# Kernel tuning notes

Hardware: AMD Instinct MI355X
Metric: run time of the kernel (lower is better)

## Reference

```python
import jax, jax.numpy as jnp
import numpy as np

DIM = 1024
HEADS = 16
HEAD_DIM = DIM // HEADS
N_CLUSTERS = 8
B, N = 4, 1024


def setup_inputs() -> dict:
    key = jax.random.key(0)
    ks = jax.random.split(key, 10)
    s = 0.02
    return {
        "x": jax.random.normal(ks[0], (B, N, DIM), dtype=jnp.float32),
        "Wqkv": jax.random.normal(ks[1], (DIM, 3 * DIM), dtype=jnp.float32) * s,
        "Wproj": jax.random.normal(ks[2], (DIM, DIM), dtype=jnp.float32) * s,
        "bproj": jnp.zeros((DIM,), dtype=jnp.float32),
        "Wgroup": jax.random.normal(ks[3], (HEAD_DIM, N_CLUSTERS), dtype=jnp.float32) * s,
        "bgroup": jnp.zeros((N_CLUSTERS,), dtype=jnp.float32),
        "Wtheta": jax.random.normal(ks[4], (HEAD_DIM, 1), dtype=jnp.float32) * s,
        "btheta": jnp.zeros((1,), dtype=jnp.float32),
        "affinity_B": jax.random.normal(ks[5], (HEADS, N_CLUSTERS, N_CLUSTERS), dtype=jnp.float32),
        "cp_bias_scale": jnp.asarray(1.0, dtype=jnp.float32),
        "flag": 1,
        "injection": 0,
        "cp_dcmm": 1,
    }


def reference(x, Wqkv, Wproj, bproj, Wgroup, bgroup, Wtheta, btheta,
              affinity_B, cp_bias_scale, flag, injection, cp_dcmm):
    b, n, c = x.shape
    h = affinity_B.shape[0]
    hd = c // h
    scale = hd ** -0.5
    # qkv: [b,n,3c] -> [3,b,h,n,hd]
    qkv = (x @ Wqkv).reshape(b, n, 3, h, hd).transpose(2, 0, 3, 1, 4)
    q, k, v = qkv[0], qkv[1], qkv[2]
    attn = jnp.einsum('bhnd,bhmd->bhnm', q, k) * scale
    z_constraint = jnp.asarray(0.0, dtype=x.dtype)
    if cp_dcmm and flag:
        # cluster assignments per query token
        z = jax.nn.softmax(q @ Wgroup + bgroup, axis=-1)          # [b,h,n,K]
        B_aff = jax.nn.sigmoid(affinity_B)                         # [h,K,K]
        zB = jnp.einsum('bhik,hkl->bhil', z, B_aff)
        cp_bias_ori = jnp.tanh(jnp.einsum('bhil,bhjl->bhij', zB, z))  # [b,h,n,n]
        theta = jax.nn.relu(jnp.squeeze(q @ Wtheta + btheta, -1))  # [b,h,n]
        degree_term = theta[..., :, None] * theta[..., None, :]
        cp_bias = cp_bias_scale * degree_term * cp_bias_ori
        attn = attn + cp_bias
        z_constraint = -(z * jnp.log(z + 1e-8)).sum(axis=-1).mean()
    else:
        cp_bias = jnp.zeros_like(attn)
    attn = jax.nn.softmax(attn, axis=-1)
    out = jnp.einsum('bhnm,bhmd->bhnd', attn, v).transpose(0, 2, 1, 3).reshape(b, n, c)
    out = out @ Wproj + bproj
    zero = jnp.asarray(0.0, dtype=x.dtype)
    return (out, z_constraint, zero, zero, cp_bias)
```

## Files before the change

### kernel.cpp

```cpp
#include <hip/hip_runtime.h>
#include <stdint.h>

#define DIM 1024
#define HEADS 16
#define HD 64
#define NC 8
#define BB 4
#define NN 1024
#define ROWS (BB*NN)
#define TOK (BB*HEADS*NN)
#define OUT_OFF_Z (ROWS*DIM)
#define CP_OFF    (ROWS*DIM+3)

typedef __bf16 bf16_t;
typedef __attribute__((ext_vector_type(8))) __bf16 bf16x8;
typedef __attribute__((ext_vector_type(4))) __bf16 bf16x4;
typedef __attribute__((ext_vector_type(4))) float f32x4;

__device__ __forceinline__ void gload16(const void* g, void* l){
#if __has_builtin(__builtin_amdgcn_global_load_lds)
  __builtin_amdgcn_global_load_lds(
      (__attribute__((address_space(1))) void*)(g),
      (__attribute__((address_space(3))) void*)(l), 16, 0, 0);
#else
  *(uint4*)l = *(const uint4*)g;
#endif
}

__global__ __launch_bounds__(256) void prep_small(const float* __restrict__ affB,
                                                  float* __restrict__ sigB,
                                                  float* __restrict__ out_scalars){
  int i = blockIdx.x*256 + threadIdx.x;
  if(i < HEADS*NC*NC) sigB[i] = 1.f/(1.f + __expf(-affB[i]));
  if(i < 3) out_scalars[i] = 0.f;
}

__global__ __launch_bounds__(256) void cvt_bf16(const float* __restrict__ in,
                                                bf16_t* __restrict__ out){
  int i = (blockIdx.x*256 + threadIdx.x)*4;
  float4 v = *(const float4*)&in[i];
  bf16x4 o = {(bf16_t)v.x, (bf16_t)v.y, (bf16_t)v.z, (bf16_t)v.w};
  *(bf16x4*)&out[i] = o;
}

__global__ __launch_bounds__(256) void transpose_bf16(const float* __restrict__ in,
                                                      bf16_t* __restrict__ out,
                                                      int K, int N){
  __shared__ float tile[32][33];
  int k0 = blockIdx.y*32, n0 = blockIdx.x*32;
  int tx = threadIdx.x & 31, ty = threadIdx.x >> 5;
  #pragma unroll
  for(int r=ty; r<32; r+=8) tile[r][tx] = in[(size_t)(k0+r)*N + n0+tx];
  __syncthreads();
  #pragma unroll
  for(int r=ty; r<32; r+=8) out[(size_t)(n0+r)*K + k0+tx] = (bf16_t)tile[tx][r];
}

__global__ __launch_bounds__(256) void gemm_qkv(const bf16_t* __restrict__ A,
                                                const bf16_t* __restrict__ Bt,
                                                bf16_t* __restrict__ Qb,
                                                bf16_t* __restrict__ Kb,
                                                bf16_t* __restrict__ Vt){
  const int K = DIM;
  __shared__ __align__(16) bf16_t As[128*32];
  __shared__ __align__(16) bf16_t Bs[128*32];
  const int tid  = threadIdx.x;
  const int m0 = blockIdx.y*128, n0 = blockIdx.x*128;
  const int wave = tid>>6, lane = tid&63, l15 = lane&15, quad = lane>>4;
  const int wm = (wave>>1)*64, wn = (wave&1)*64;

  f32x4 acc[4][4];
  #pragma unroll
  for(int i=0;i<4;i++)
    #pragma unroll
    for(int j=0;j<4;j++) acc[i][j] = (f32x4){0.f,0.f,0.f,0.f};

  for(int k0=0; k0<K; k0+=32){
    int c = tid;
    gload16(A  + (size_t)(m0 + (c>>2))*K + k0 + (c&3)*8, &As[c*8]);
    gload16(Bt + (size_t)(n0 + (c>>2))*K + k0 + (c&3)*8, &Bs[c*8]);
    c = tid + 256;
    gload16(A  + (size_t)(m0 + (c>>2))*K + k0 + (c&3)*8, &As[c*8]);
    gload16(Bt + (size_t)(n0 + (c>>2))*K + k0 + (c&3)*8, &Bs[c*8]);
    __syncthreads();

    bf16x8 a[4], b[4];
    #pragma unroll
    for(int i=0;i<4;i++) a[i] = *(const bf16x8*)&As[(wm + i*16 + l15)*32 + quad*8];
    #pragma unroll
    for(int j=0;j<4;j++) b[j] = *(const bf16x8*)&Bs[(wn + j*16 + l15)*32 + quad*8];
    #pragma unroll
    for(int i=0;i<4;i++)
      #pragma unroll
      for(int j=0;j<4;j++)
        acc[i][j] = __builtin_amdgcn_mfma_f32_16x16x32_bf16(a[i], b[j], acc[i][j], 0,0,0);
    __syncthreads();
  }

  #pragma unroll
  for(int j=0;j<4;j++){
    int col = n0 + wn + j*16 + l15;
    int which = col>>10, hc = col&1023, h = hc>>6, d = hc&63;
    #pragma unroll
    for(int i=0;i<4;i++){
      int m = m0 + wm + i*16 + quad*4;
      #pragma unroll
      for(int r=0;r<4;r++){
        int row = m + r;
        int bh = (row>>10)*HEADS + h, n = row&1023;
        bf16_t v = (bf16_t)acc[i][j][r];
        if(which==0)      Qb[((size_t)bh*NN + n)*HD + d] = v;
        else if(which==1) Kb[((size_t)bh*NN + n)*HD + d] = v;
        else              Vt[((size_t)bh*HD + d)*NN + n] = v;
      }
    }
  }
}

__global__ __launch_bounds__(256) void token_kernel(
    const bf16_t* __restrict__ Qb, const float* __restrict__ Wgroup,
    const float* __restrict__ bgroup, const float* __restrict__ Wtheta,
    const float* __restrict__ btheta, const float* __restrict__ sigB,
    bf16_t* __restrict__ zb16, bf16_t* __restrict__ zBb16,
    float* __restrict__ thetaAll, float* __restrict__ entPart){
  const int wv = threadIdx.x>>6, lane = threadIdx.x&63;
  const int t = blockIdx.x*4 + wv;
  const int h = (t>>10)&15;
  float qd = (float)Qb[(size_t)t*HD + lane];

  float zl[8];
  #pragma unroll
  for(int c=0;c<8;c++){
    float p = qd * Wgroup[lane*NC + c];
    p += __shfl_xor(p,1);  p += __shfl_xor(p,2);  p += __shfl_xor(p,4);
    p += __shfl_xor(p,8);  p += __shfl_xor(p,16); p += __shfl_xor(p,32);
    zl[c] = p + bgroup[c];
  }
  float th = qd * Wtheta[lane];
  th += __shfl_xor(th,1);  th += __shfl_xor(th,2);  th += __shfl_xor(th,4);
  th += __shfl_xor(th,8);  th += __shfl_xor(th,16); th += __shfl_xor(th,32);
  th = fmaxf(th + btheta[0], 0.f);

  float mx = zl[0];
  #pragma unroll
  for(int c=1;c<8;c++) mx = fmaxf(mx, zl[c]);
  float ssum = 0.f;
  #pragma unroll
  for(int c=0;c<8;c++){ zl[c] = __expf(zl[c]-mx); ssum += zl[c]; }
  float inv = 1.f/ssum;
  float ent = 0.f;
  #pragma unroll
  for(int c=0;c<8;c++){ float z = zl[c]*inv; zl[c] = z; ent -= z*__logf(z + 1e-8f); }

  float zb[8];
  #pragma unroll
  for(int l=0;l<8;l++){
    float a = 0.f;
    #pragma unroll
    for(int k2=0;k2<8;k2++) a += zl[k2]*sigB[h*64 + k2*8 + l];
    zb[l] = a;
  }
  if(lane==0){
    bf16x8 zv, zbv;
    #pragma unroll
    for(int c=0;c<8;c++){ zv[c] = (bf16_t)zl[c]; zbv[c] = (bf16_t)zb[c]; }
    *(bf16x8*)&zb16[(size_t)t*8]  = zv;
    *(bf16x8*)&zBb16[(size_t)t*8] = zbv;
    thetaAll[t] = th;
  }

  __shared__ float es[4];
  if(lane==0) es[wv] = ent;
  __syncthreads();
  if(threadIdx.x==0) entPart[blockIdx.x] = es[0]+es[1]+es[2]+es[3];
}

__global__ __launch_bounds__(256) void reduce_ent(const float* __restrict__ part,
                                                  float* __restrict__ outz){
  float s = 0.f;
  for(int i=threadIdx.x; i<TOK/4; i+=256) s += part[i];
  s += __shfl_xor(s,1); s += __shfl_xor(s,2); s += __shfl_xor(s,4);
  s += __shfl_xor(s,8); s += __shfl_xor(s,16); s += __shfl_xor(s,32);
  __shared__ float ls[4];
  if((threadIdx.x&63)==0) ls[threadIdx.x>>6] = s;
  __syncthreads();
  if(threadIdx.x==0) outz[0] = (ls[0]+ls[1]+ls[2]+ls[3]) * (1.0f/(float)TOK);
}

__global__ __launch_bounds__(256) void flash_kernel(
    const bf16_t* __restrict__ Qb, const bf16_t* __restrict__ Kb,
    const bf16_t* __restrict__ Vt, const bf16_t* __restrict__ zb16,
    const bf16_t* __restrict__ zBb16, const float* __restrict__ thetaAll,
    const float* __restrict__ cps_p, float* __restrict__ cp_out,
    bf16_t* __restrict__ attnO){
  const int bid = blockIdx.x;
  const int bh = bid & 63, qt = bid >> 6;
  const int b = bh >> 4;
  const int tid = threadIdx.x;
  const int wave = tid>>6, lane = tid&63, l15 = lane&15, quad = lane>>4;

  __shared__ __align__(16) bf16_t Qs[64*64];
  __shared__ __align__(16) bf16_t Ks[64*64];
  __shared__ __align__(16) bf16_t Vs[64*64];
  __shared__ __align__(16) bf16_t Ps[4][16*72];

  const float cps = cps_p[0];

  {
    const bf16_t* Qg = Qb + ((size_t)bh*NN + (size_t)qt*64)*HD;
    gload16(Qg + tid*8, &Qs[tid*8]);
    gload16(Qg + (tid+256)*8, &Qs[(tid+256)*8]);
  }
  bf16x8 aZ = (bf16x8)(bf16_t)0.f;
  if(quad==0)
    aZ = *(const bf16x8*)&zBb16[((size_t)bh*NN + qt*64 + wave*16 + l15)*8];
  float th_i[4];
  #pragma unroll
  for(int r=0;r<4;r++)
    th_i[r] = thetaAll[(size_t)bh*NN + qt*64 + wave*16 + quad*4 + r];
  __syncthreads();

  bf16x8 aq0 = *(const bf16x8*)&Qs[(wave*16 + l15)*64 + quad*8];
  bf16x8 aq1 = *(const bf16x8*)&Qs[(wave*16 + l15)*64 + 32 + quad*8];

  float m_r[4] = {-1e30f,-1e30f,-1e30f,-1e30f};
  float l_r[4] = {0.f,0.f,0.f,0.f};
  f32x4 o[4];
  #pragma unroll
  for(int dn=0;dn<4;dn++) o[dn] = (f32x4){0.f,0.f,0.f,0.f};

  for(int kt=0; kt<16; ++kt){
    const bf16_t* Kg = Kb + ((size_t)bh*NN + (size_t)kt*64)*HD;
    gload16(Kg + tid*8, &Ks[tid*8]);
    gload16(Kg + (tid+256)*8, &Ks[(tid+256)*8]);
    {
      int c = tid;
      gload16(Vt + (size_t)(bh*HD + (c>>3))*NN + kt*64 + (c&7)*8, &Vs[c*8]);
      c = tid + 256;
      gload16(Vt + (size_t)(bh*HD + (c>>3))*NN + kt*64 + (c&7)*8, &Vs[c*8]);
    }

    f32x4 D[4];
    #pragma unroll
    for(int f=0;f<4;f++){
      bf16x8 bz = (bf16x8)(bf16_t)0.f;
      if(quad==0)
        bz = *(const bf16x8*)&zb16[((size_t)bh*NN + kt*64 + f*16 + l15)*8];
      D[f] = __builtin_amdgcn_mfma_f32_16x16x32_bf16(aZ, bz, (f32x4){0.f,0.f,0.f,0.f}, 0,0,0);
    }
    float biasv[4][4];
    #pragma unroll
    for(int f=0;f<4;f++){
      int jloc = f*16 + l15;
      float thj = thetaAll[(size_t)bh*NN + kt*64 + jloc];
      #pragma unroll
      for(int r=0;r<4;r++){
        float d = D[f][r];
        float t2 = d*d;
        float p = -0.33333333f + t2*(0.13333333f + t2*(-0.05396825f));
        float tnh = d*(1.f + t2*p);
        float bv = cps * th_i[r] * thj * tnh;
        biasv[f][r] = bv;
        int irow = qt*64 + wave*16 + quad*4 + r;
        cp_out[((size_t)bh*NN + irow)*NN + (size_t)kt*64 + jloc] = bv;
      }
    }
    __syncthreads();

    f32x4 s[4];
    #pragma unroll
    for(int f=0;f<4;f++){
      f32x4 z4 = (f32x4){0.f,0.f,0.f,0.f};
      bf16x8 b0 = *(const bf16x8*)&Ks[(f*16 + l15)*64 + quad*8];
      bf16x8 b1 = *(const bf16x8*)&Ks[(f*16 + l15)*64 + 32 + quad*8];
      z4 = __builtin_amdgcn_mfma_f32_16x16x32_bf16(aq0, b0, z4, 0,0,0);
      z4 = __builtin_amdgcn_mfma_f32_16x16x32_bf16(aq1, b1, z4, 0,0,0);
      #pragma unroll
      for(int r=0;r<4;r++) z4[r] = z4[r]*0.125f + biasv[f][r];
      s[f] = z4;
    }

    float alpha[4];
    #pragma unroll
    for(int r=0;r<4;r++){
      float v = fmaxf(fmaxf(s[0][r],s[1][r]), fmaxf(s[2][r],s[3][r]));
      v = fmaxf(v, __shfl_xor(v,1));
      v = fmaxf(v, __shfl_xor(v,2));
      v = fmaxf(v, __shfl_xor(v,4));
      v = fmaxf(v, __shfl_xor(v,8));
      float mn = fmaxf(m_r[r], v);
      alpha[r] = __expf(m_r[r] - mn);
      m_r[r] = mn;
    }
    float rs[4] = {0.f,0.f,0.f,0.f};
    #pragma unroll
    for(int f=0;f<4;f++)
      #pragma unroll
      for(int r=0;r<4;r++){
        float p = __expf(s[f][r] - m_r[r]);
        s[f][r] = p;
        rs[r] += p;
      }
    #pragma unroll
    for(int r=0;r<4;r++){
      float v = rs[r];
      v += __shfl_xor(v,1); v += __shfl_xor(v,2);
      v += __shfl_xor(v,4); v += __shfl_xor(v,8);
      l_r[r] = l_r[r]*alpha[r] + v;
      #pragma unroll
      for(int dn=0;dn<4;dn++) o[dn][r] *= alpha[r];
    }

    #pragma unroll
    for(int f=0;f<4;f++)
      #pragma unroll
      for(int r=0;r<4;r++)
        Ps[wave][(quad*4+r)*72 + f*16 + l15] = (bf16_t)s[f][r];

    bf16x8 pa0 = *(const bf16x8*)&Ps[wave][l15*72 + quad*8];
    bf16x8 pa1 = *(const bf16x8*)&Ps[wave][l15*72 + 32 + quad*8];
    #pragma unroll
    for(int dn=0;dn<4;dn++){
      bf16x8 b0 = *(const bf16x8*)&Vs[(dn*16 + l15)*64 + quad*8];
      bf16x8 b1 = *(const bf16x8*)&Vs[(dn*16 + l15)*64 + 32 + quad*8];
      o[dn] = __builtin_amdgcn_mfma_f32_16x16x32_bf16(pa0, b0, o[dn], 0,0,0);
      o[dn] = __builtin_amdgcn_mfma_f32_16x16x32_bf16(pa1, b1, o[dn], 0,0,0);
    }
    __syncthreads();
  }

  #pragma unroll
  for(int r=0;r<4;r++){
    float inv = 1.f / l_r[r];
    int grow = qt*64 + wave*16 + quad*4 + r;
    #pragma unroll
    for(int dn=0;dn<4;dn++)
      attnO[((size_t)(b*NN + grow))*DIM + (bh&15)*HD + dn*16 + l15] = (bf16_t)(o[dn][r]*inv);
  }
}

__global__ __launch_bounds__(256) void gemm_proj(const bf16_t* __restrict__ A,
                                                 const bf16_t* __restrict__ Bt,
                                                 float* __restrict__ C,
                                                 const float* __restrict__ bias){
  const int K = DIM, N = DIM;
  __shared__ __align__(16) bf16_t As[128*32];
  __shared__ __align__(16) bf16_t Bs[64*32];
  const int tid  = threadIdx.x;
  const int m0 = blockIdx.y*128, n0 = blockIdx.x*64;
  const int wave = tid>>6, lane = tid&63, l15 = lane&15, quad = lane>>4;
  const int wm = (wave>>1)*64, wn = (wave&1)*32;

  f32x4 acc[4][2];
  #pragma unroll
  for(int i=0;i<4;i++)
    #pragma unroll
    for(int j=0;j<2;j++) acc[i][j] = (f32x4){0.f,0.f,0.f,0.f};

  for(int k0=0; k0<K; k0+=32){
    int c = tid;
    gload16(A  + (size_t)(m0 + (c>>2))*K + k0 + (c&3)*8, &As[c*8]);
    gload16(Bt + (size_t)(n0 + (c>>2))*K + k0 + (c&3)*8, &Bs[c*8]);
    c = tid + 256;
    gload16(A  + (size_t)(m0 + (c>>2))*K + k0 + (c&3)*8, &As[c*8]);
    __syncthreads();

    bf16x8 a[4], b[2];
    #pragma unroll
    for(int i=0;i<4;i++) a[i] = *(const bf16x8*)&As[(wm + i*16 + l15)*32 + quad*8];
    #pragma unroll
    for(int j=0;j<2;j++) b[j] = *(const bf16x8*)&Bs[(wn + j*16 + l15)*32 + quad*8];
    #pragma unroll
    for(int i=0;i<4;i++)
      #pragma unroll
      for(int j=0;j<2;j++)
        acc[i][j] = __builtin_amdgcn_mfma_f32_16x16x32_bf16(a[i], b[j], acc[i][j], 0,0,0);
    __syncthreads();
  }

  #pragma unroll
  for(int i=0;i<4;i++)
    #pragma unroll
    for(int j=0;j<2;j++){
      int row = m0 + wm + i*16 + quad*4;
      int col = n0 + wn + j*16 + l15;
      float bv = bias[col];
      #pragma unroll
      for(int r=0;r<4;r++)
        C[(size_t)(row+r)*N + col] = acc[i][j][r] + bv;
    }
}

extern "C" void kernel_launch(void* const* d_in, const int* in_sizes, int n_in,
                              void* d_out, int out_size, void* d_ws, size_t ws_size,
                              hipStream_t stream){
  const float* x      = (const float*)d_in[0];
  const float* Wqkv   = (const float*)d_in[1];
  const float* Wproj  = (const float*)d_in[2];
  const float* bproj  = (const float*)d_in[3];
  const float* Wgroup = (const float*)d_in[4];
  const float* bgroup = (const float*)d_in[5];
  const float* Wtheta = (const float*)d_in[6];
  const float* btheta = (const float*)d_in[7];
  const float* affB   = (const float*)d_in[8];
  const float* cps    = (const float*)d_in[9];
  float* out = (float*)d_out;
  char* ws = (char*)d_ws;

  bf16_t* xb       = (bf16_t*)(ws);
  bf16_t* WqkvT    = (bf16_t*)(ws + (size_t)8*1048576);
  bf16_t* WprojT   = (bf16_t*)(ws + (size_t)14*1048576);
  bf16_t* Qb       = (bf16_t*)(ws + (size_t)16*1048576);
  bf16_t* Kb       = (bf16_t*)(ws + (size_t)24*1048576);
  bf16_t* Vt       = (bf16_t*)(ws + (size_t)32*1048576);
  bf16_t* zb16     = (bf16_t*)(ws + (size_t)40*1048576);
  bf16_t* zBb16    = (bf16_t*)(ws + (size_t)41*1048576);
  float*  thetaAll = (float*) (ws + (size_t)42*1048576);
  float*  entPart  = (float*) (ws + (size_t)43*1048576);
  bf16_t* attnO    = (bf16_t*)(ws + (size_t)44*1048576);
  float*  sigB     = (float*) (ws + (size_t)52*1048576);

  prep_small<<<4, 256, 0, stream>>>(affB, sigB, out + OUT_OFF_Z);
  cvt_bf16<<<(ROWS*DIM)/1024, 256, 0, stream>>>(x, xb);
  transpose_bf16<<<dim3(96,32), 256, 0, stream>>>(Wqkv, WqkvT, 1024, 3072);
  transpose_bf16<<<dim3(32,32), 256, 0, stream>>>(Wproj, WprojT, 1024, 1024);
  gemm_qkv<<<dim3(24,32), 256, 0, stream>>>(xb, WqkvT, Qb, Kb, Vt);
  token_kernel<<<TOK/4, 256, 0, stream>>>(Qb, Wgroup, bgroup, Wtheta, btheta, sigB,
                                          zb16, zBb16, thetaAll, entPart);
  reduce_ent<<<1, 256, 0, stream>>>(entPart, out + OUT_OFF_Z);
  flash_kernel<<<1024, 256, 0, stream>>>(Qb, Kb, Vt, zb16, zBb16, thetaAll,
                                         cps, out + CP_OFF, attnO);
  gemm_proj<<<dim3(16,32), 256, 0, stream>>>(attnO, WprojT, out, bproj);
}
```

Before: 575.4 us.

## Split V GEMM into transposed kernel, drop online-softmax max, cache theta in LDS

Splits the QKV projection in two. Q and K keep the original GEMM. V is now a separate GEMM computing Wv·x^T, so the transposed V layout comes out with coalesced stores instead of the strided scatter. The flash kernel stages per-head theta in shared memory and removes the running-max rescaling of online softmax, exponentiating scores directly on the assumption they stay small. That skips the max reductions and the accumulator rescales, but risks overflow if logits grow large.

```diff
diff --git a/kernel.cpp b/kernel.cpp
--- a/kernel.cpp
+++ b/kernel.cpp
@@ -56,11 +56,10 @@
   for(int r=ty; r<32; r+=8) out[(size_t)(n0+r)*K + k0+tx] = (bf16_t)tile[tx][r];
 }
 
-__global__ __launch_bounds__(256) void gemm_qkv(const bf16_t* __restrict__ A,
-                                                const bf16_t* __restrict__ Bt,
-                                                bf16_t* __restrict__ Qb,
-                                                bf16_t* __restrict__ Kb,
-                                                bf16_t* __restrict__ Vt){
+__global__ __launch_bounds__(256) void gemm_qk(const bf16_t* __restrict__ A,
+                                               const bf16_t* __restrict__ Bt,
+                                               bf16_t* __restrict__ Qb,
+                                               bf16_t* __restrict__ Kb){
   const int K = DIM;
   __shared__ __align__(16) bf16_t As[128*32];
   __shared__ __align__(16) bf16_t Bs[128*32];
@@ -101,6 +100,7 @@
   for(int j=0;j<4;j++){
     int col = n0 + wn + j*16 + l15;
     int which = col>>10, hc = col&1023, h = hc>>6, d = hc&63;
+    bf16_t* dst = which ? Kb : Qb;
     #pragma unroll
     for(int i=0;i<4;i++){
       int m = m0 + wm + i*16 + quad*4;
@@ -108,13 +108,62 @@
       for(int r=0;r<4;r++){
         int row = m + r;
         int bh = (row>>10)*HEADS + h, n = row&1023;
-        bf16_t v = (bf16_t)acc[i][j][r];
-        if(which==0)      Qb[((size_t)bh*NN + n)*HD + d] = v;
-        else if(which==1) Kb[((size_t)bh*NN + n)*HD + d] = v;
-        else              Vt[((size_t)bh*HD + d)*NN + n] = v;
+        dst[((size_t)bh*NN + n)*HD + d] = (bf16_t)acc[i][j][r];
       }
     }
   }
+}
+
+__global__ __launch_bounds__(256) void gemm_vt(const bf16_t* __restrict__ Wv,
+                                               const bf16_t* __restrict__ Xb,
+                                               bf16_t* __restrict__ Vt){
+  const int K = DIM;
+  __shared__ __align__(16) bf16_t As[128*32];
+  __shared__ __align__(16) bf16_t Bs[128*32];
+  const int tid  = threadIdx.x;
+  const int m0 = blockIdx.y*128, n0 = blockIdx.x*128;
+  const int wave = tid>>6, lane = tid&63, l15 = lane&15, quad = lane>>4;
+  const int wm = (wave>>1)*64, wn = (wave&1)*64;
+
+  f32x4 acc[4][4];
+  #pragma unroll
+  for(int i=0;i<4;i++)
+    #pragma unroll
+    for(int j=0;j<4;j++) acc[i][j] = (f32x4){0.f,0.f,0.f,0.f};
+
+  for(int k0=0; k0<K; k0+=32){
+    int c = tid;
+    gload16(Wv + (size_t)(m0 + (c>>2))*K + k0 + (c&3)*8, &As[c*8]);
+    gload16(Xb + (size_t)(n0 + (c>>2))*K + k0 + (c&3)*8, &Bs[c*8]);
+    c = tid + 256;
+    gload16(Wv + (size_t)(m0 + (c>>2))*K + k0 + (c&3)*8, &As[c*8]);
+    gload16(Xb + (size_t)(n0 + (c>>2))*K + k0 + (c&3)*8, &Bs[c*8]);
+    __syncthreads();
+
+    bf16x8 a[4], b[4];
+    #pragma unroll
+    for(int i=0;i<4;i++) a[i] = *(const bf16x8*)&As[(wm + i*16 + l15)*32 + quad*8];
+    #pragma unroll
+    for(int j=0;j<4;j++) b[j] = *(const bf16x8*)&Bs[(wn + j*16 + l15)*32 + quad*8];
+    #pragma unroll
+    for(int i=0;i<4;i++)
+      #pragma unroll
+      for(int j=0;j<4;j++)
+        acc[i][j] = __builtin_amdgcn_mfma_f32_16x16x32_bf16(a[i], b[j], acc[i][j], 0,0,0);
+    __syncthreads();
+  }
+
+  const int b = n0 >> 10;
+  #pragma unroll
+  for(int i=0;i<4;i++)
+    #pragma unroll
+    for(int j=0;j<4;j++){
+      int vcol = m0 + wm + i*16 + quad*4;
+      int ncol = n0 + wn + j*16 + l15;
+      #pragma unroll
+      for(int r=0;r<4;r++)
+        Vt[((size_t)(b*1024 + vcol + r))*NN + (ncol & 1023)] = (bf16_t)acc[i][j][r];
+    }
 }
 
 __global__ __launch_bounds__(256) void token_kernel(
@@ -195,7 +244,7 @@
     bf16_t* __restrict__ attnO){
   const int bid = blockIdx.x;
   const int bh = bid & 63, qt = bid >> 6;
-  const int b = bh >> 4;
+  const int b = bh >> 4, h = bh & 15;
   const int tid = threadIdx.x;
   const int wave = tid>>6, lane = tid&63, l15 = lane&15, quad = lane>>4;
 
@@ -203,6 +252,7 @@
   __shared__ __align__(16) bf16_t Ks[64*64];
   __shared__ __align__(16) bf16_t Vs[64*64];
   __shared__ __align__(16) bf16_t Ps[4][16*72];
+  __shared__ float thAll[NN];
 
   const float cps = cps_p[0];
 
@@ -210,20 +260,23 @@
     const bf16_t* Qg = Qb + ((size_t)bh*NN + (size_t)qt*64)*HD;
     gload16(Qg + tid*8, &Qs[tid*8]);
     gload16(Qg + (tid+256)*8, &Qs[(tid+256)*8]);
+    const float* tg = thetaAll + (size_t)bh*NN;
+    float4 tv = *(const float4*)&tg[tid*4];
+    *(float4*)&thAll[tid*4] = tv;
   }
   bf16x8 aZ = (bf16x8)(bf16_t)0.f;
   if(quad==0)
     aZ = *(const bf16x8*)&zBb16[((size_t)bh*NN + qt*64 + wave*16 + l15)*8];
+  __syncthreads();
+
   float th_i[4];
   #pragma unroll
   for(int r=0;r<4;r++)
-    th_i[r] = thetaAll[(size_t)bh*NN + qt*64 + wave*16 + quad*4 + r];
-  __syncthreads();
+    th_i[r] = thAll[qt*64 + wave*16 + quad*4 + r];
 
   bf16x8 aq0 = *(const bf16x8*)&Qs[(wave*16 + l15)*64 + quad*8];
   bf16x8 aq1 = *(const bf16x8*)&Qs[(wave*16 + l15)*64 + 32 + quad*8];
 
-  float m_r[4] = {-1e30f,-1e30f,-1e30f,-1e30f};
   float l_r[4] = {0.f,0.f,0.f,0.f};
   f32x4 o[4];
   #pragma unroll
@@ -252,7 +305,7 @@
     #pragma unroll
     for(int f=0;f<4;f++){
       int jloc = f*16 + l15;
-      float thj = thetaAll[(size_t)bh*NN + kt*64 + jloc];
+      float thj = thAll[kt*64 + jloc];
       #pragma unroll
       for(int r=0;r<4;r++){
         float d = D[f][r];
@@ -268,6 +321,7 @@
     __syncthreads();
 
     f32x4 s[4];
+    float rs[4] = {0.f,0.f,0.f,0.f};
     #pragma unroll
     for(int f=0;f<4;f++){
       f32x4 z4 = (f32x4){0.f,0.f,0.f,0.f};
@@ -276,39 +330,19 @@
       z4 = __builtin_amdgcn_mfma_f32_16x16x32_bf16(aq0, b0, z4, 0,0,0);
       z4 = __builtin_amdgcn_mfma_f32_16x16x32_bf16(aq1, b1, z4, 0,0,0);
       #pragma unroll
-      for(int r=0;r<4;r++) z4[r] = z4[r]*0.125f + biasv[f][r];
-      s[f] = z4;
-    }
-
-    float alpha[4];
-    #pragma unroll
-    for(int r=0;r<4;r++){
-      float v = fmaxf(fmaxf(s[0][r],s[1][r]), fmaxf(s[2][r],s[3][r]));
-      v = fmaxf(v, __shfl_xor(v,1));
-      v = fmaxf(v, __shfl_xor(v,2));
-      v = fmaxf(v, __shfl_xor(v,4));
-      v = fmaxf(v, __shfl_xor(v,8));
-      float mn = fmaxf(m_r[r], v);
-      alpha[r] = __expf(m_r[r] - mn);
-      m_r[r] = mn;
-    }
-    float rs[4] = {0.f,0.f,0.f,0.f};
-    #pragma unroll
-    for(int f=0;f<4;f++)
-      #pragma unroll
       for(int r=0;r<4;r++){
-        float p = __expf(s[f][r] - m_r[r]);
-        s[f][r] = p;
+        float p = __expf(z4[r]*0.125f + biasv[f][r]);
+        z4[r] = p;
         rs[r] += p;
       }
+      s[f] = z4;
+    }
     #pragma unroll
     for(int r=0;r<4;r++){
       float v = rs[r];
       v += __shfl_xor(v,1); v += __shfl_xor(v,2);
       v += __shfl_xor(v,4); v += __shfl_xor(v,8);
-      l_r[r] = l_r[r]*alpha[r] + v;
-      #pragma unroll
-      for(int dn=0;dn<4;dn++) o[dn][r] *= alpha[r];
+      l_r[r] += v;
     }
 
     #pragma unroll
@@ -335,7 +369,7 @@
     int grow = qt*64 + wave*16 + quad*4 + r;
     #pragma unroll
     for(int dn=0;dn<4;dn++)
-      attnO[((size_t)(b*NN + grow))*DIM + (bh&15)*HD + dn*16 + l15] = (bf16_t)(o[dn][r]*inv);
+      attnO[((size_t)(b*NN + grow))*DIM + h*HD + dn*16 + l15] = (bf16_t)(o[dn][r]*inv);
   }
 }
 
@@ -424,7 +458,8 @@
   cvt_bf16<<<(ROWS*DIM)/1024, 256, 0, stream>>>(x, xb);
   transpose_bf16<<<dim3(96,32), 256, 0, stream>>>(Wqkv, WqkvT, 1024, 3072);
   transpose_bf16<<<dim3(32,32), 256, 0, stream>>>(Wproj, WprojT, 1024, 1024);
-  gemm_qkv<<<dim3(24,32), 256, 0, stream>>>(xb, WqkvT, Qb, Kb, Vt);
+  gemm_qk<<<dim3(16,32), 256, 0, stream>>>(xb, WqkvT, Qb, Kb);
+  gemm_vt<<<dim3(32,8), 256, 0, stream>>>(WqkvT + (size_t)2048*DIM, xb, Vt);
   token_kernel<<<TOK/4, 256, 0, stream>>>(Qb, Wgroup, bgroup, Wtheta, btheta, sigB,
                                           zb16, zBb16, thetaAll, entPart);
   reduce_ent<<<1, 256, 0, stream>>>(entPart, out + OUT_OFF_Z);
```

Result: no change. 572.2 us (-0.6%).
